# Kernel optimization log

Hardware: AMD Instinct MI355X
Metric: run time of the kernel (lower is better)

## Reference

```python
import jax, jax.numpy as jnp
import numpy as np

DEPTH = 10
LAMDA = 1e-3
EPS = 1e-7


def setup_inputs() -> dict:
    key = jax.random.key(0)
    k1, k2, k3, k4 = jax.random.split(key, 4)
    B, D, O = 16384, 512, 256
    N = 2 ** DEPTH - 1        # inner nodes
    L = 2 ** DEPTH            # leaves
    data = jax.random.normal(k1, (B, D), jnp.float32)
    # small scale on W keeps sigmoid away from saturation (like nn.Linear init)
    W = jax.random.normal(k2, (N, D + 1), jnp.float32) * 0.02
    beta = jax.random.normal(k3, (N,), jnp.float32)
    param = jax.random.normal(k4, (L, O), jnp.float32)
    return {"data": data, "W": W, "beta": beta, "param": param}


def reference(data, W, beta, param):
    B = data.shape[0]
    L = param.shape[0]
    # _data_augment_: prepend constant 1 as bias feature -> [B, D+1]
    x = jnp.concatenate([jnp.ones((B, 1), data.dtype), data], axis=1)
    # inner_nodes: sigmoid(beta * linear(x)) -> [B, N]
    p = jax.nn.sigmoid(beta * (x @ W.T))
    # per-node (go-left, go-right) probabilities -> [B, N, 2]
    path_prob = jnp.stack([p, 1.0 - p], axis=2)

    mu = jnp.ones((B, 1), data.dtype)          # path prob of root
    penalty = jnp.asarray(0.0, data.dtype)
    begin = 0
    for layer in range(DEPTH):                  # fixed small loop over depth
        n = 2 ** layer
        pp = path_prob[:, begin:begin + n, :].reshape(B, 2 * n)  # [B, 2n]
        mu_rep = jnp.repeat(mu, 2, axis=1)                        # [B, 2n]
        # vectorized form of the per-node penalty loop
        alpha = jnp.sum(pp * mu_rep, axis=0) / (jnp.sum(mu_rep, axis=0) + EPS)
        alpha = jnp.clip(alpha, EPS, 1.0 - EPS)
        coeff = LAMDA * (2.0 ** (-layer))
        penalty = penalty - coeff * 0.5 * jnp.sum(jnp.log(alpha) + jnp.log(1.0 - alpha))
        mu = mu_rep * pp
        begin += n

    # mu: [B, leaf_num]; leaf_nodes: mu @ softmax(param)
    dist = jax.nn.softmax(param, axis=1)       # [L, O]
    output = mu @ dist                          # [B, O]
    # greatest_path_probability: hard argmax leaf (one-hot @ dist == gather)
    ids = jnp.argmax(mu, axis=1)
    prediction = dist[ids]                      # [B, O]
    # LogProb=True
    return (jnp.log(prediction), jnp.log(output), penalty, W)
```

## Files before the change

### kernel.cpp

```cpp
#include <hip/hip_runtime.h>
#include <hip/hip_bf16.h>

#define B_ROWS 16384
#define DDIM   512
#define NNODES 1023
#define NLEAF  1024
#define ODIM   256
#define LAMDA  1e-3
#define EPSV   1e-7f

typedef __bf16 bf16x8v __attribute__((ext_vector_type(8)));
typedef _Float16 f16x8 __attribute__((ext_vector_type(8)));
typedef float  f32x16v __attribute__((ext_vector_type(16)));

__device__ __forceinline__ float bf2f(unsigned short u) {
    return __uint_as_float(((unsigned)u) << 16);
}

__device__ __forceinline__ void gload16h(const _Float16* g, _Float16* l) {
    __builtin_amdgcn_global_load_lds(
        (const __attribute__((address_space(1))) unsigned int*)g,
        (__attribute__((address_space(3))) unsigned int*)l, 16, 0, 0);
}
__device__ __forceinline__ void gload16b(const __hip_bfloat16* g, __hip_bfloat16* l) {
    __builtin_amdgcn_global_load_lds(
        (const __attribute__((address_space(1))) unsigned int*)g,
        (__attribute__((address_space(3))) unsigned int*)l, 16, 0, 0);
}

__global__ __launch_bounds__(256)
void prep_all(const float* __restrict__ data, const float* __restrict__ W,
              const float* __restrict__ param,
              _Float16* __restrict__ Dh, _Float16* __restrict__ Dl,
              _Float16* __restrict__ Wh, _Float16* __restrict__ Wl,
              float* __restrict__ outW,
              float* __restrict__ logdist, __hip_bfloat16* __restrict__ DT2,
              float* __restrict__ leafsum)
{
    __shared__ float red[4], red2[4];
    if (blockIdx.x < 4096) {
        int idx = blockIdx.x * 256 + threadIdx.x;
        int b  = idx >> 6;
        int k8 = idx & 63;
        const float4 v0 = *reinterpret_cast<const float4*>(&data[(size_t)b * DDIM + k8 * 8]);
        const float4 v1 = *reinterpret_cast<const float4*>(&data[(size_t)b * DDIM + k8 * 8 + 4]);
        float a[8] = {v0.x, v0.y, v0.z, v0.w, v1.x, v1.y, v1.z, v1.w};
        __align__(16) _Float16 h[8], l[8];
#pragma unroll
        for (int j = 0; j < 8; ++j) {
            h[j] = (_Float16)a[j];
            l[j] = (_Float16)((a[j] - (float)h[j]) * 2048.f);
        }
        int by = b >> 8, tl = (b >> 5) & 7, ln = (b & 31) | ((k8 & 1) << 5), ks = k8 >> 1;
        size_t off = ((((size_t)by * 32 + ks) * 8 + tl) * 64 + ln) * 8;
        *reinterpret_cast<ulonglong2*>(&Dh[off]) = *reinterpret_cast<const ulonglong2*>(h);
        *reinterpret_cast<ulonglong2*>(&Dl[off]) = *reinterpret_cast<const ulonglong2*>(l);
    } else if (blockIdx.x < 4352) {
        int idx = (blockIdx.x - 4096) * 256 + threadIdx.x;
        int t  = idx & 255;
        int ks = (idx >> 8) & 31;
        int nb = idx >> 13;
        int tm = t >> 6, ln = t & 63;
        int node = nb * 128 + tm * 32 + (ln & 31);
        int k = ks * 16 + (ln >> 5) * 8;
        __align__(16) _Float16 h[8], l[8];
        if (node < NNODES) {
#pragma unroll
            for (int j = 0; j < 8; ++j) {
                float a = W[(size_t)node * 513 + 1 + k + j];
                h[j] = (_Float16)a;
                l[j] = (_Float16)((a - (float)h[j]) * 2048.f);
            }
        } else {
#pragma unroll
            for (int j = 0; j < 8; ++j) { h[j] = (_Float16)0.f; l[j] = (_Float16)0.f; }
        }
        size_t off = (size_t)idx * 8;
        *reinterpret_cast<ulonglong2*>(&Wh[off]) = *reinterpret_cast<const ulonglong2*>(h);
        *reinterpret_cast<ulonglong2*>(&Wl[off]) = *reinterpret_cast<const ulonglong2*>(l);
    } else if (blockIdx.x < 6404) {
        int i = (blockIdx.x - 4352) * 256 + threadIdx.x;
        if (i < NNODES * 513) outW[i] = W[i];
    } else if (blockIdx.x < 7428) {
        int l = blockIdx.x - 6404;
        int o = threadIdx.x;
        float x = param[(size_t)l * ODIM + o];
        float m = x;
#pragma unroll
        for (int s = 1; s < 64; s <<= 1) m = fmaxf(m, __shfl_xor(m, s, 64));
        if ((o & 63) == 0) red[o >> 6] = m;
        __syncthreads();
        m = fmaxf(fmaxf(red[0], red[1]), fmaxf(red[2], red[3]));
        float e = expf(x - m);
        float s = e;
#pragma unroll
        for (int k = 1; k < 64; k <<= 1) s += __shfl_xor(s, k, 64);
        if ((o & 63) == 0) red2[o >> 6] = s;
        __syncthreads();
        s = red2[0] + red2[1] + red2[2] + red2[3];
        float d = e / s;
        logdist[(size_t)l * ODIM + o] = logf(d);
        int kc = l >> 4, kk = l & 15;
        int lane = (o & 31) | ((kk >> 3) << 5);
        DT2[(((size_t)kc * 8 + (o >> 5)) * 64 + lane) * 8 + (kk & 7)] = __float2bfloat16(d);
    } else {
        float4 z = {0.f, 0.f, 0.f, 0.f};
        *reinterpret_cast<float4*>(&leafsum[threadIdx.x * 4]) = z;
    }
}

__global__ __launch_bounds__(512, 4)
void gemm1_mfma(const _Float16* __restrict__ Wh, const _Float16* __restrict__ Wl,
                const _Float16* __restrict__ Dh, const _Float16* __restrict__ Dl,
                const float* __restrict__ W, const float* __restrict__ beta,
                float* __restrict__ PT)
{
    __shared__ _Float16 lds[2][8192];
    const int tid = threadIdx.x;
    const int lane = tid & 63;
    const int wv = tid >> 6;
    const int wm = wv & 1, wn = wv >> 1;
    const int id = blockIdx.x;
    const int xcd = id & 7, slot = id >> 3;
    const int bx = slot & 7;
    const int by = xcd * 16 + (slot >> 3);
    const int by256 = by >> 1;
    const int tlb = (by & 1) * 4;

    const int q  = tid & 255;
    const int qt = q >> 6, qn = q & 63;
    const _Float16* Wsel = (tid < 256) ? Wh : Wl;
    const _Float16* Dsel = (tid < 256) ? Dh : Dl;
    const _Float16* wsrc = Wsel + (size_t)bx * 65536 + qt * 512 + qn * 8;
    const _Float16* dsrc = Dsel + (size_t)by256 * 131072 + (tlb + qt) * 512 + qn * 8;

    f32x16v acc_h[2] = {};
    f32x16v acc_l[2] = {};

#define STAGE(buf, ks) do { \
        gload16h(wsrc + (size_t)(ks) * 2048, &lds[buf][tid * 8]); \
        gload16h(dsrc + (size_t)(ks) * 4096, &lds[buf][4096 + tid * 8]); \
    } while (0)

    STAGE(0, 0);
    for (int t = 0; t < 32; ++t) {
        const int cur = t & 1;
        if (t < 31) {
            STAGE(cur ^ 1, t + 1);
            asm volatile("s_waitcnt vmcnt(2)" ::: "memory");
        } else {
            asm volatile("s_waitcnt vmcnt(0)" ::: "memory");
        }
        __builtin_amdgcn_s_barrier();

        f16x8 ah[2], al[2], bh, bl;
#pragma unroll
        for (int i = 0; i < 2; ++i) {
            int ao = ((wm * 2 + i) * 64 + lane) * 8;
            ah[i] = *reinterpret_cast<const f16x8*>(&lds[cur][ao]);
            al[i] = *reinterpret_cast<const f16x8*>(&lds[cur][2048 + ao]);
        }
        {
            int bo = (wn * 64 + lane) * 8;
            bh = *reinterpret_cast<const f16x8*>(&lds[cur][4096 + bo]);
            bl = *reinterpret_cast<const f16x8*>(&lds[cur][6144 + bo]);
        }
        __builtin_amdgcn_s_setprio(1);
#pragma unroll
        for (int i = 0; i < 2; ++i) {
            acc_h[i] = __builtin_amdgcn_mfma_f32_32x32x16_f16(ah[i], bh, acc_h[i], 0, 0, 0);
            acc_l[i] = __builtin_amdgcn_mfma_f32_32x32x16_f16(ah[i], bl, acc_l[i], 0, 0, 0);
            acc_l[i] = __builtin_amdgcn_mfma_f32_32x32x16_f16(al[i], bh, acc_l[i], 0, 0, 0);
        }
        __builtin_amdgcn_s_setprio(0);
        asm volatile("s_waitcnt lgkmcnt(0)" ::: "memory");
        __builtin_amdgcn_s_barrier();
    }
#undef STAGE

#pragma unroll
    for (int i = 0; i < 2; ++i) {
#pragma unroll
        for (int r = 0; r < 16; ++r) {
            int node = bx * 128 + wm * 64 + i * 32 + ((r & 3) + 8 * (r >> 2) + 4 * (lane >> 5));
            if (node < NNODES) {
                float w0 = W[(size_t)node * 513];
                float bt = beta[node];
                float z = acc_h[i][r] + acc_l[i][r] * 4.8828125e-4f;
                float s = bt * (z + w0);
                float p = 1.f / (1.f + expf(-s));
                PT[(size_t)node * B_ROWS + by * 128 + wn * 32 + (lane & 31)] = p;
            }
        }
    }
}

__global__ __launch_bounds__(256, 4)
void tree_pass(const float* __restrict__ PT,
               __hip_bfloat16* __restrict__ MU2,
               float* __restrict__ pval,
               int*   __restrict__ pidx,
               float* __restrict__ leafsum)
{
    __shared__ float cs[32][257];
    __shared__ float ps[32][8];
    const int tid = threadIdx.x;
    const int rb = blockIdx.x & 63;
    const int g  = blockIdx.x >> 6;
    const int b  = rb * 256 + tid;

    const int c4 = 15 + g;
    const int n3 = (c4 - 1) >> 1;
    const int n2 = (n3 - 1) >> 1;
    const int n1 = (n2 - 1) >> 1;
    const float pc4 = PT[(size_t)c4 * B_ROWS + b];
    const float pn3 = PT[(size_t)n3 * B_ROWS + b];
    const float pn2 = PT[(size_t)n2 * B_ROWS + b];
    const float pn1 = PT[(size_t)n1 * B_ROWS + b];
    const float pn0 = PT[b];
    float pre = ((c4 & 1) ? pn3 : 1.f - pn3)
              * ((n3 & 1) ? pn2 : 1.f - pn2)
              * ((n2 & 1) ? pn1 : 1.f - pn1)
              * ((n1 & 1) ? pn0 : 1.f - pn0);
    float root[2] = { pre * pc4, pre * (1.f - pc4) };

    __align__(16) __hip_bfloat16 mbv[64];
    float bestv = -1.f; int besti = 0;
#pragma unroll
    for (int ss = 0; ss < 2; ++ss) {
        const int t = 2 * g + ss;
        float s[32];
#pragma unroll
        for (int u = 1; u < 32; ++u) {
            int lvl = 31 - __clz(u);
            int node = ((32 << lvl) - 1) + t * (1 << lvl) + (u - (1 << lvl));
            s[u] = PT[(size_t)node * B_ROWS + b];
        }
        float w[64];
        w[1] = root[ss];
#pragma unroll
        for (int u = 1; u < 32; ++u) {
            w[2 * u]     = w[u] * s[u];
            w[2 * u + 1] = w[u] * (1.f - s[u]);
        }
#pragma unroll
        for (int q = 0; q < 32; ++q) {
            float lv = w[32 + q];
            mbv[ss * 32 + q] = __float2bfloat16(lv);
            if (lv > bestv) { bestv = lv; besti = t * 32 + q; }
        }
#pragma unroll
        for (int q = 0; q < 32; ++q) cs[q][tid] = w[32 + q];
        __syncthreads();
        {
            const int q = tid & 31, seg = tid >> 5;
            float sum = 0.f;
#pragma unroll
            for (int r = 0; r < 32; ++r) sum += cs[q][seg * 32 + r];
            ps[q][seg] = sum;
        }
        __syncthreads();
        if (tid < 32) {
            float tot = 0.f;
#pragma unroll
            for (int sg = 0; sg < 8; ++sg) tot += ps[tid][sg];
            atomicAdd(&leafsum[t * 32 + tid], tot);
        }
        __syncthreads();
    }
    {
        const int mb_ = b >> 7, mt_ = (b >> 5) & 3, lnlo = b & 31;
        const ulonglong2* src = reinterpret_cast<const ulonglong2*>(mbv);
#pragma unroll
        for (int c = 0; c < 4; ++c) {
            size_t base16 = (((size_t)mb_ * 64 + g * 4 + c) * 4 + mt_) * 64;
            *reinterpret_cast<ulonglong2*>(&MU2[(base16 + lnlo) * 8])      = src[c * 2];
            *reinterpret_cast<ulonglong2*>(&MU2[(base16 + 32 + lnlo) * 8]) = src[c * 2 + 1];
        }
    }
    pval[(size_t)g * B_ROWS + b] = bestv;
    pidx[(size_t)g * B_ROWS + b] = besti;
}

__global__ __launch_bounds__(256)
void tail_kernel(const __hip_bfloat16* __restrict__ MU2,
                 const __hip_bfloat16* __restrict__ DT2,
                 float* __restrict__ out1,
                 const float* __restrict__ pval, const int* __restrict__ pidx,
                 const float* __restrict__ logdist, float* __restrict__ out0,
                 const float* __restrict__ leafsum, float* __restrict__ out_pen)
{
    __shared__ __hip_bfloat16 ldsA[2][2048];
    __shared__ __hip_bfloat16 ldsB[2][8192];
    __shared__ float M[2048];
    __shared__ double dred[256];
    __shared__ int sid[64];
    const int tid = threadIdx.x;

    if (blockIdx.x >= 512) {
        for (int i = tid; i < 1024; i += 256) M[1024 + i] = leafsum[i];
        __syncthreads();
        for (int n = 512; n >= 1; n >>= 1) {
            for (int u = n + tid; u < 2 * n; u += 256) M[u] = M[2 * u] + M[2 * u + 1];
            __syncthreads();
        }
        double acc = 0.0;
        for (int u = 2 + tid; u < 2048; u += 256) {
            int lvl = 31 - __clz(u);
            float a = M[u] / (M[u >> 1] + EPSV);
            a = fminf(fmaxf(a, EPSV), 1.f - EPSV);
            float term = logf(a) + logf(1.f - a);
            acc -= ldexp((double)LAMDA * 0.5, 1 - lvl) * (double)term;
        }
        dred[tid] = acc;
        __syncthreads();
        for (int s = 128; s > 0; s >>= 1) {
            if (tid < s) dred[tid] += dred[tid + s];
            __syncthreads();
        }
        if (tid == 0) out_pen[0] = (float)dred[0];
        return;
    }
    if (blockIdx.x >= 256) {
        const int blk = blockIdx.x - 256;
        if (tid < 64) {
            int row = blk * 64 + tid;
            float bv = -1.f; int bi = 0;
            for (int g = 0; g < 16; ++g) {
                float v = pval[(size_t)g * B_ROWS + row];
                if (v > bv) { bv = v; bi = pidx[(size_t)g * B_ROWS + row]; }
            }
            sid[tid] = bi;
        }
        __syncthreads();
        for (int rr = 0; rr < 64; ++rr) {
            int id = sid[rr];
            out0[(size_t)(blk * 64 + rr) * ODIM + tid] = logdist[(size_t)id * ODIM + tid];
        }
        return;
    }
    const int lane = tid & 63;
    const int w = tid >> 6;
    const int blk = blockIdx.x;
    const int m0 = blk * 64;
    const int mb = blk >> 1;
    const int mtbase = (blk & 1) * 2;
    const int s_kcl = tid >> 7, s_mti = (tid >> 6) & 1, s_ln = tid & 63;

    f32x16v acc[2][2] = {};

#define STAGE2(buf, kc0) do { \
        size_t sa16 = (((size_t)mb * 64 + (kc0) + s_kcl) * 4 + mtbase + s_mti) * 64 + s_ln; \
        gload16b(MU2 + sa16 * 8, &ldsA[buf][tid * 8]); \
        gload16b(DT2 + ((size_t)(kc0) * 512 + tid) * 8,             &ldsB[buf][tid * 8]); \
        gload16b(DT2 + ((size_t)(kc0) * 512 + 256 + tid) * 8,       &ldsB[buf][2048 + tid * 8]); \
        gload16b(DT2 + ((size_t)((kc0) + 1) * 512 + tid) * 8,       &ldsB[buf][4096 + tid * 8]); \
        gload16b(DT2 + ((size_t)((kc0) + 1) * 512 + 256 + tid) * 8, &ldsB[buf][6144 + tid * 8]); \
    } while (0)

    STAGE2(0, 0);
    for (int it = 0; it < 32; ++it) {
        const int cur = it & 1;
        if (it + 1 < 32) {
            STAGE2(cur ^ 1, 2 * (it + 1));
            asm volatile("s_waitcnt vmcnt(5)" ::: "memory");
        } else {
            asm volatile("s_waitcnt vmcnt(0)" ::: "memory");
        }
        __builtin_amdgcn_s_barrier();
        bf16x8v a[2][2], bb[2][2];
#pragma unroll
        for (int kcl = 0; kcl < 2; ++kcl)
#pragma unroll
            for (int i = 0; i < 2; ++i) {
                a[kcl][i]  = *reinterpret_cast<const bf16x8v*>(&ldsA[cur][((kcl * 2 + i) * 64 + lane) * 8]);
                bb[kcl][i] = *reinterpret_cast<const bf16x8v*>(&ldsB[cur][((kcl * 8 + 2 * w + i) * 64 + lane) * 8]);
            }
        __builtin_amdgcn_s_setprio(1);
#pragma unroll
        for (int kcl = 0; kcl < 2; ++kcl)
#pragma unroll
            for (int i = 0; i < 2; ++i)
#pragma unroll
                for (int j = 0; j < 2; ++j)
                    acc[i][j] = __builtin_amdgcn_mfma_f32_32x32x16_bf16(a[kcl][i], bb[kcl][j], acc[i][j], 0, 0, 0);
        __builtin_amdgcn_s_setprio(0);
        asm volatile("s_waitcnt lgkmcnt(0)" ::: "memory");
        __builtin_amdgcn_s_barrier();
    }
#undef STAGE2
#pragma unroll
    for (int i = 0; i < 2; ++i)
#pragma unroll
        for (int j = 0; j < 2; ++j)
#pragma unroll
            for (int r = 0; r < 16; ++r) {
                int row = m0 + i * 32 + (r & 3) + 8 * (r >> 2) + 4 * (lane >> 5);
                int col = w * 64 + j * 32 + (lane & 31);
                out1[(size_t)row * ODIM + col] = logf(acc[i][j][r]);
            }
}

extern "C" void kernel_launch(void* const* d_in, const int* in_sizes, int n_in,
                              void* d_out, int out_size, void* d_ws, size_t ws_size,
                              hipStream_t stream)
{
    (void)in_sizes; (void)n_in; (void)out_size; (void)ws_size;
    const float* data  = (const float*)d_in[0];
    const float* W     = (const float*)d_in[1];
    const float* beta  = (const float*)d_in[2];
    const float* param = (const float*)d_in[3];
    float* out = (float*)d_out;

    char* ws = (char*)d_ws;
    size_t off = 0;
    float* PT = (float*)(ws + off);                   off += (size_t)NNODES * B_ROWS * 4;
    char* X = ws + off;                               off += 2 * 1048576 + 2 * 16777216;
    _Float16* Wh = (_Float16*)(X);
    _Float16* Wl = (_Float16*)(X + 1048576);
    _Float16* Dh = (_Float16*)(X + 2 * 1048576);
    _Float16* Dl = (_Float16*)(X + 2 * 1048576 + 16777216);
    __hip_bfloat16* MU2 = (__hip_bfloat16*)(X + 2 * 1048576);
    __hip_bfloat16* DT2 = (__hip_bfloat16*)(ws + off); off += (size_t)ODIM * NLEAF * 2;
    float* logdist = (float*)(ws + off);              off += (size_t)NLEAF * ODIM * 4;
    float* leafsum = (float*)(ws + off);              off += (size_t)NLEAF * 4;
    float* pval    = (float*)(ws + off);              off += (size_t)16 * B_ROWS * 4;
    int*   pidx    = (int*)(ws + off);                off += (size_t)16 * B_ROWS * 4;

    float* out_logpred = out;
    float* out_logout  = out + (size_t)B_ROWS * ODIM;
    float* out_pen     = out + 2 * (size_t)B_ROWS * ODIM;
    float* out_W       = out_pen + 1;

    prep_all<<<7429, 256, 0, stream>>>(data, W, param, Dh, Dl, Wh, Wl, out_W,
                                       logdist, DT2, leafsum);

    gemm1_mfma<<<1024, 512, 0, stream>>>(Wh, Wl, Dh, Dl, W, beta, PT);

    tree_pass<<<1024, 256, 0, stream>>>(PT, MU2, pval, pidx, leafsum);

    tail_kernel<<<513, 256, 0, stream>>>(MU2, DT2, out_logout,
                                         pval, pidx, logdist, out_logpred,
                                         leafsum, out_pen);
}
```

Measured before the change: 137.6 us.

## Fuse tree pass into leaf GEMM tail, keeping mu rows in LDS

Merges the tree traversal kernel and the output GEMM/argmax-gather kernel into one kernel. Each block computes leaf path probabilities for its 64 rows directly into a large LDS buffer, then runs the MFMA GEMM against the leaf distribution from LDS with a triple-buffered B stream. The penalty reduction moves to a separate single-block kernel. This removes the global round trip of the mu matrix and the per-group argmax partials. The cost is only 256 blocks at one block per CU, with a ~132KB LDS footprint, which reduces parallelism and latency hiding in the tree phase.

```diff
diff --git a/kernel.cpp b/kernel.cpp
--- a/kernel.cpp
+++ b/kernel.cpp
@@ -195,210 +195,198 @@
     }
 }
 
-__global__ __launch_bounds__(256, 4)
-void tree_pass(const float* __restrict__ PT,
-               __hip_bfloat16* __restrict__ MU2,
-               float* __restrict__ pval,
-               int*   __restrict__ pidx,
-               float* __restrict__ leafsum)
+__global__ __launch_bounds__(256, 1)
+void fused_tail(const float* __restrict__ PT,
+                const __hip_bfloat16* __restrict__ DT2,
+                const float* __restrict__ logdist,
+                float* __restrict__ out0,
+                float* __restrict__ out1,
+                float* __restrict__ leafsum)
 {
-    __shared__ float cs[32][257];
-    __shared__ float ps[32][8];
+    __shared__ __hip_bfloat16 Abuf[64 * 1032];
+    __shared__ __hip_bfloat16 ldsB[3][4096];
+    __shared__ float amaxv[4][64];
+    __shared__ int   amaxi[4][64];
+    __shared__ int   sid[64];
+
     const int tid = threadIdx.x;
-    const int rb = blockIdx.x & 63;
-    const int g  = blockIdx.x >> 6;
-    const int b  = rb * 256 + tid;
-
-    const int c4 = 15 + g;
-    const int n3 = (c4 - 1) >> 1;
-    const int n2 = (n3 - 1) >> 1;
-    const int n1 = (n2 - 1) >> 1;
-    const float pc4 = PT[(size_t)c4 * B_ROWS + b];
-    const float pn3 = PT[(size_t)n3 * B_ROWS + b];
-    const float pn2 = PT[(size_t)n2 * B_ROWS + b];
-    const float pn1 = PT[(size_t)n1 * B_ROWS + b];
-    const float pn0 = PT[b];
-    float pre = ((c4 & 1) ? pn3 : 1.f - pn3)
-              * ((n3 & 1) ? pn2 : 1.f - pn2)
-              * ((n2 & 1) ? pn1 : 1.f - pn1)
-              * ((n1 & 1) ? pn0 : 1.f - pn0);
-    float root[2] = { pre * pc4, pre * (1.f - pc4) };
-
-    __align__(16) __hip_bfloat16 mbv[64];
-    float bestv = -1.f; int besti = 0;
-#pragma unroll
-    for (int ss = 0; ss < 2; ++ss) {
-        const int t = 2 * g + ss;
-        float s[32];
-#pragma unroll
-        for (int u = 1; u < 32; ++u) {
-            int lvl = 31 - __clz(u);
-            int node = ((32 << lvl) - 1) + t * (1 << lvl) + (u - (1 << lvl));
-            s[u] = PT[(size_t)node * B_ROWS + b];
-        }
-        float w[64];
-        w[1] = root[ss];
-#pragma unroll
-        for (int u = 1; u < 32; ++u) {
-            w[2 * u]     = w[u] * s[u];
-            w[2 * u + 1] = w[u] * (1.f - s[u]);
-        }
-#pragma unroll
-        for (int q = 0; q < 32; ++q) {
-            float lv = w[32 + q];
-            mbv[ss * 32 + q] = __float2bfloat16(lv);
-            if (lv > bestv) { bestv = lv; besti = t * 32 + q; }
-        }
-#pragma unroll
-        for (int q = 0; q < 32; ++q) cs[q][tid] = w[32 + q];
-        __syncthreads();
-        {
-            const int q = tid & 31, seg = tid >> 5;
-            float sum = 0.f;
-#pragma unroll
-            for (int r = 0; r < 32; ++r) sum += cs[q][seg * 32 + r];
-            ps[q][seg] = sum;
-        }
-        __syncthreads();
-        if (tid < 32) {
-            float tot = 0.f;
-#pragma unroll
-            for (int sg = 0; sg < 8; ++sg) tot += ps[tid][sg];
-            atomicAdd(&leafsum[t * 32 + tid], tot);
-        }
-        __syncthreads();
-    }
+    const int lane = tid & 63;
+    const int wvi = tid >> 6;
+    const int m0 = blockIdx.x * 64;
+
     {
-        const int mb_ = b >> 7, mt_ = (b >> 5) & 3, lnlo = b & 31;
-        const ulonglong2* src = reinterpret_cast<const ulonglong2*>(mbv);
-#pragma unroll
-        for (int c = 0; c < 4; ++c) {
-            size_t base16 = (((size_t)mb_ * 64 + g * 4 + c) * 4 + mt_) * 64;
-            *reinterpret_cast<ulonglong2*>(&MU2[(base16 + lnlo) * 8])      = src[c * 2];
-            *reinterpret_cast<ulonglong2*>(&MU2[(base16 + 32 + lnlo) * 8]) = src[c * 2 + 1];
-        }
-    }
-    pval[(size_t)g * B_ROWS + b] = bestv;
-    pidx[(size_t)g * B_ROWS + b] = besti;
-}
-
-__global__ __launch_bounds__(256)
-void tail_kernel(const __hip_bfloat16* __restrict__ MU2,
-                 const __hip_bfloat16* __restrict__ DT2,
-                 float* __restrict__ out1,
-                 const float* __restrict__ pval, const int* __restrict__ pidx,
-                 const float* __restrict__ logdist, float* __restrict__ out0,
-                 const float* __restrict__ leafsum, float* __restrict__ out_pen)
-{
-    __shared__ __hip_bfloat16 ldsA[2][2048];
-    __shared__ __hip_bfloat16 ldsB[2][8192];
-    __shared__ float M[2048];
-    __shared__ double dred[256];
-    __shared__ int sid[64];
-    const int tid = threadIdx.x;
-
-    if (blockIdx.x >= 512) {
-        for (int i = tid; i < 1024; i += 256) M[1024 + i] = leafsum[i];
-        __syncthreads();
-        for (int n = 512; n >= 1; n >>= 1) {
-            for (int u = n + tid; u < 2 * n; u += 256) M[u] = M[2 * u] + M[2 * u + 1];
-            __syncthreads();
-        }
-        double acc = 0.0;
-        for (int u = 2 + tid; u < 2048; u += 256) {
-            int lvl = 31 - __clz(u);
-            float a = M[u] / (M[u >> 1] + EPSV);
-            a = fminf(fmaxf(a, EPSV), 1.f - EPSV);
-            float term = logf(a) + logf(1.f - a);
-            acc -= ldexp((double)LAMDA * 0.5, 1 - lvl) * (double)term;
-        }
-        dred[tid] = acc;
-        __syncthreads();
-        for (int s = 128; s > 0; s >>= 1) {
-            if (tid < s) dred[tid] += dred[tid + s];
-            __syncthreads();
-        }
-        if (tid == 0) out_pen[0] = (float)dred[0];
-        return;
-    }
-    if (blockIdx.x >= 256) {
-        const int blk = blockIdx.x - 256;
-        if (tid < 64) {
-            int row = blk * 64 + tid;
-            float bv = -1.f; int bi = 0;
-            for (int g = 0; g < 16; ++g) {
-                float v = pval[(size_t)g * B_ROWS + row];
-                if (v > bv) { bv = v; bi = pidx[(size_t)g * B_ROWS + row]; }
+        const int r  = tid & 63;
+        const int gg = tid >> 6;
+        const int b  = m0 + r;
+        const float pn0 = PT[b];
+        float bestv = -1.f; int besti = 0;
+
+        for (int pp = 0; pp < 4; ++pp) {
+            const int g = gg * 4 + pp;
+            const int c4 = 15 + g;
+            const int n3 = (c4 - 1) >> 1;
+            const int n2 = (n3 - 1) >> 1;
+            const int n1 = (n2 - 1) >> 1;
+            const float pc4 = PT[(size_t)c4 * B_ROWS + b];
+            const float pn3 = PT[(size_t)n3 * B_ROWS + b];
+            const float pn2 = PT[(size_t)n2 * B_ROWS + b];
+            const float pn1 = PT[(size_t)n1 * B_ROWS + b];
+            float pre = ((c4 & 1) ? pn3 : 1.f - pn3)
+                      * ((n3 & 1) ? pn2 : 1.f - pn2)
+                      * ((n2 & 1) ? pn1 : 1.f - pn1)
+                      * ((n1 & 1) ? pn0 : 1.f - pn0);
+            float root[2] = { pre * pc4, pre * (1.f - pc4) };
+
+#pragma unroll
+            for (int ss = 0; ss < 2; ++ss) {
+                const int t = 2 * g + ss;
+                float s[32];
+#pragma unroll
+                for (int u = 1; u < 32; ++u) {
+                    int lvl = 31 - __clz(u);
+                    int node = ((32 << lvl) - 1) + t * (1 << lvl) + (u - (1 << lvl));
+                    s[u] = PT[(size_t)node * B_ROWS + b];
+                }
+                float w[64];
+                w[1] = root[ss];
+#pragma unroll
+                for (int u = 1; u < 32; ++u) {
+                    w[2 * u]     = w[u] * s[u];
+                    w[2 * u + 1] = w[u] * (1.f - s[u]);
+                }
+                __align__(16) __hip_bfloat16 mb32[32];
+#pragma unroll
+                for (int qq = 0; qq < 32; ++qq) {
+                    float lv = w[32 + qq];
+                    mb32[qq] = __float2bfloat16(lv);
+                    if (lv > bestv) { bestv = lv; besti = t * 32 + qq; }
+                }
+                const ulonglong2* src = reinterpret_cast<const ulonglong2*>(mb32);
+#pragma unroll
+                for (int c = 0; c < 4; ++c)
+                    *reinterpret_cast<ulonglong2*>(&Abuf[(size_t)r * 1032 + t * 32 + c * 8]) = src[c];
             }
-            sid[tid] = bi;
-        }
-        __syncthreads();
-        for (int rr = 0; rr < 64; ++rr) {
-            int id = sid[rr];
-            out0[(size_t)(blk * 64 + rr) * ODIM + tid] = logdist[(size_t)id * ODIM + tid];
-        }
-        return;
-    }
-    const int lane = tid & 63;
-    const int w = tid >> 6;
-    const int blk = blockIdx.x;
-    const int m0 = blk * 64;
-    const int mb = blk >> 1;
-    const int mtbase = (blk & 1) * 2;
-    const int s_kcl = tid >> 7, s_mti = (tid >> 6) & 1, s_ln = tid & 63;
+        }
+        amaxv[gg][r] = bestv;
+        amaxi[gg][r] = besti;
+    }
+    __syncthreads();
+
+#define STAGEB(buf, kc) do { \
+        gload16b(DT2 + (size_t)(kc) * 4096 + tid * 8,        &ldsB[buf][tid * 8]); \
+        gload16b(DT2 + (size_t)(kc) * 4096 + 2048 + tid * 8, &ldsB[buf][2048 + tid * 8]); \
+    } while (0)
+
+    STAGEB(0, 0);
+    STAGEB(1, 1);
+
+    {
+        const int chunk = tid >> 1, half = tid & 1;
+        float cs8[8] = {0.f, 0.f, 0.f, 0.f, 0.f, 0.f, 0.f, 0.f};
+        for (int rr = 0; rr < 32; ++rr) {
+            int row = half * 32 + rr;
+            ulonglong2 u = *reinterpret_cast<const ulonglong2*>(&Abuf[(size_t)row * 1032 + chunk * 8]);
+            const unsigned short* hs = reinterpret_cast<const unsigned short*>(&u);
+#pragma unroll
+            for (int j = 0; j < 8; ++j) cs8[j] += bf2f(hs[j]);
+        }
+#pragma unroll
+        for (int j = 0; j < 8; ++j) cs8[j] += __shfl_xor(cs8[j], 1, 64);
+        if (half == 0) {
+#pragma unroll
+            for (int j = 0; j < 8; ++j) atomicAdd(&leafsum[chunk * 8 + j], cs8[j]);
+        }
+    }
+    if (tid < 64) {
+        float bv = -1.f; int bi = 0;
+#pragma unroll
+        for (int gg2 = 0; gg2 < 4; ++gg2) {
+            float v = amaxv[gg2][tid];
+            if (v > bv) { bv = v; bi = amaxi[gg2][tid]; }
+        }
+        sid[tid] = bi;
+    }
+    __syncthreads();
 
     f32x16v acc[2][2] = {};
-
-#define STAGE2(buf, kc0) do { \
-        size_t sa16 = (((size_t)mb * 64 + (kc0) + s_kcl) * 4 + mtbase + s_mti) * 64 + s_ln; \
-        gload16b(MU2 + sa16 * 8, &ldsA[buf][tid * 8]); \
-        gload16b(DT2 + ((size_t)(kc0) * 512 + tid) * 8,             &ldsB[buf][tid * 8]); \
-        gload16b(DT2 + ((size_t)(kc0) * 512 + 256 + tid) * 8,       &ldsB[buf][2048 + tid * 8]); \
-        gload16b(DT2 + ((size_t)((kc0) + 1) * 512 + tid) * 8,       &ldsB[buf][4096 + tid * 8]); \
-        gload16b(DT2 + ((size_t)((kc0) + 1) * 512 + 256 + tid) * 8, &ldsB[buf][6144 + tid * 8]); \
-    } while (0)
-
-    STAGE2(0, 0);
-    for (int it = 0; it < 32; ++it) {
-        const int cur = it & 1;
-        if (it + 1 < 32) {
-            STAGE2(cur ^ 1, 2 * (it + 1));
-            asm volatile("s_waitcnt vmcnt(5)" ::: "memory");
+    int buf = 0;
+    for (int kc = 0; kc < 64; ++kc) {
+        if (kc < 62) {
+            int sb = (buf >= 1) ? buf - 1 : 2;
+            STAGEB(sb, kc + 2);
+            asm volatile("s_waitcnt vmcnt(4)" ::: "memory");
+        } else if (kc == 62) {
+            asm volatile("s_waitcnt vmcnt(2)" ::: "memory");
         } else {
             asm volatile("s_waitcnt vmcnt(0)" ::: "memory");
         }
         __builtin_amdgcn_s_barrier();
-        bf16x8v a[2][2], bb[2][2];
-#pragma unroll
-        for (int kcl = 0; kcl < 2; ++kcl)
-#pragma unroll
-            for (int i = 0; i < 2; ++i) {
-                a[kcl][i]  = *reinterpret_cast<const bf16x8v*>(&ldsA[cur][((kcl * 2 + i) * 64 + lane) * 8]);
-                bb[kcl][i] = *reinterpret_cast<const bf16x8v*>(&ldsB[cur][((kcl * 8 + 2 * w + i) * 64 + lane) * 8]);
-            }
+
+        bf16x8v a[2], bb[2];
+#pragma unroll
+        for (int i = 0; i < 2; ++i)
+            a[i] = *reinterpret_cast<const bf16x8v*>(
+                &Abuf[(size_t)(i * 32 + (lane & 31)) * 1032 + kc * 16 + (lane >> 5) * 8]);
+#pragma unroll
+        for (int j = 0; j < 2; ++j)
+            bb[j] = *reinterpret_cast<const bf16x8v*>(&ldsB[buf][((2 * wvi + j) * 64 + lane) * 8]);
+
         __builtin_amdgcn_s_setprio(1);
 #pragma unroll
-        for (int kcl = 0; kcl < 2; ++kcl)
-#pragma unroll
-            for (int i = 0; i < 2; ++i)
-#pragma unroll
-                for (int j = 0; j < 2; ++j)
-                    acc[i][j] = __builtin_amdgcn_mfma_f32_32x32x16_bf16(a[kcl][i], bb[kcl][j], acc[i][j], 0, 0, 0);
+        for (int i = 0; i < 2; ++i)
+#pragma unroll
+            for (int j = 0; j < 2; ++j)
+                acc[i][j] = __builtin_amdgcn_mfma_f32_32x32x16_bf16(a[i], bb[j], acc[i][j], 0, 0, 0);
         __builtin_amdgcn_s_setprio(0);
         asm volatile("s_waitcnt lgkmcnt(0)" ::: "memory");
         __builtin_amdgcn_s_barrier();
-    }
-#undef STAGE2
+        buf = (buf == 2) ? 0 : buf + 1;
+    }
+#undef STAGEB
+
 #pragma unroll
     for (int i = 0; i < 2; ++i)
 #pragma unroll
         for (int j = 0; j < 2; ++j)
 #pragma unroll
-            for (int r = 0; r < 16; ++r) {
-                int row = m0 + i * 32 + (r & 3) + 8 * (r >> 2) + 4 * (lane >> 5);
-                int col = w * 64 + j * 32 + (lane & 31);
-                out1[(size_t)row * ODIM + col] = logf(acc[i][j][r]);
+            for (int rr = 0; rr < 16; ++rr) {
+                int row = m0 + i * 32 + (rr & 3) + 8 * (rr >> 2) + 4 * (lane >> 5);
+                int col = wvi * 64 + j * 32 + (lane & 31);
+                out1[(size_t)row * ODIM + col] = logf(acc[i][j][rr]);
             }
+    for (int rr = 0; rr < 64; ++rr) {
+        int id = sid[rr];
+        out0[(size_t)(m0 + rr) * ODIM + tid] = logdist[(size_t)id * ODIM + tid];
+    }
+}
+
+__global__ __launch_bounds__(256)
+void penalty_kernel(const float* __restrict__ leafsum, float* __restrict__ out_pen)
+{
+    __shared__ float M[2048];
+    __shared__ double dred[256];
+    int tid = threadIdx.x;
+    for (int i = tid; i < 1024; i += 256) M[1024 + i] = leafsum[i];
+    __syncthreads();
+    for (int n = 512; n >= 1; n >>= 1) {
+        for (int u = n + tid; u < 2 * n; u += 256) M[u] = M[2 * u] + M[2 * u + 1];
+        __syncthreads();
+    }
+    double acc = 0.0;
+    for (int u = 2 + tid; u < 2048; u += 256) {
+        int lvl = 31 - __clz(u);
+        float a = M[u] / (M[u >> 1] + EPSV);
+        a = fminf(fmaxf(a, EPSV), 1.f - EPSV);
+        float term = logf(a) + logf(1.f - a);
+        acc -= ldexp((double)LAMDA * 0.5, 1 - lvl) * (double)term;
+    }
+    dred[tid] = acc;
+    __syncthreads();
+    for (int s = 128; s > 0; s >>= 1) {
+        if (tid < s) dred[tid] += dred[tid + s];
+        __syncthreads();
+    }
+    if (tid == 0) out_pen[0] = (float)dred[0];
 }
 
 extern "C" void kernel_launch(void* const* d_in, const int* in_sizes, int n_in,
@@ -420,12 +408,9 @@
     _Float16* Wl = (_Float16*)(X + 1048576);
     _Float16* Dh = (_Float16*)(X + 2 * 1048576);
     _Float16* Dl = (_Float16*)(X + 2 * 1048576 + 16777216);
-    __hip_bfloat16* MU2 = (__hip_bfloat16*)(X + 2 * 1048576);
     __hip_bfloat16* DT2 = (__hip_bfloat16*)(ws + off); off += (size_t)ODIM * NLEAF * 2;
     float* logdist = (float*)(ws + off);              off += (size_t)NLEAF * ODIM * 4;
     float* leafsum = (float*)(ws + off);              off += (size_t)NLEAF * 4;
-    float* pval    = (float*)(ws + off);              off += (size_t)16 * B_ROWS * 4;
-    int*   pidx    = (int*)(ws + off);                off += (size_t)16 * B_ROWS * 4;
 
     float* out_logpred = out;
     float* out_logout  = out + (size_t)B_ROWS * ODIM;
@@ -437,9 +422,8 @@
 
     gemm1_mfma<<<1024, 512, 0, stream>>>(Wh, Wl, Dh, Dl, W, beta, PT);
 
-    tree_pass<<<1024, 256, 0, stream>>>(PT, MU2, pval, pidx, leafsum);
-
-    tail_kernel<<<513, 256, 0, stream>>>(MU2, DT2, out_logout,
-                                         pval, pidx, logdist, out_logpred,
-                                         leafsum, out_pen);
-}
+    fused_tail<<<256, 256, 0, stream>>>(PT, DT2, logdist, out_logpred,
+                                        out_logout, leafsum);
+
+    penalty_kernel<<<1, 256, 0, stream>>>(leafsum, out_pen);
+}
```

Result: slower. 185.8 us (+35.0%).
